# Kernel optimization log

Hardware: AMD Instinct MI355X
Metric: run time of the kernel (lower is better)

The kernel has to match this reference:

```python
import jax, jax.numpy as jnp
import numpy as np

L, D_IN, D, H, FF, C = 6, 64, 512, 8, 2048, 5
HD = D // H
LN_EPS = 1e-5


def _ln(x, g, b):
    mu = jnp.mean(x, axis=-1, keepdims=True)
    var = jnp.mean((x - mu) ** 2, axis=-1, keepdims=True)
    return (x - mu) * jax.lax.rsqrt(var + LN_EPS) * g + b


def setup_inputs() -> dict:
    key = jax.random.key(0)
    ks = iter(jax.random.split(key, 64))
    s = 0.02

    def w(shape):
        return (jax.random.normal(next(ks), shape, dtype=jnp.float32) * s)

    inp = {
        "src": jax.random.normal(next(ks), (8, 1024, D_IN), dtype=jnp.float32),
        "key_padding_mask": jnp.zeros((8, 1024), dtype=bool),
        "embed_W": w((D, D_IN)), "embed_b": jnp.zeros((D,), jnp.float32),
        # stacked per-layer params (torch Linear convention: W is [out, in])
        "Wq": w((L, D, D)), "bq": jnp.zeros((L, D), jnp.float32),
        "Wk": w((L, D, D)), "bk": jnp.zeros((L, D), jnp.float32),
        "Wv": w((L, D, D)), "bv": jnp.zeros((L, D), jnp.float32),
        "Wo": w((L, D, D)), "bo": jnp.zeros((L, D), jnp.float32),
        "W1": w((L, FF, D)), "b1": jnp.zeros((L, FF), jnp.float32),
        "W2": w((L, D, FF)), "b2": jnp.zeros((L, D), jnp.float32),
        "ln1_g": jnp.ones((L, D), jnp.float32), "ln1_b": jnp.zeros((L, D), jnp.float32),
        "ln2_g": jnp.ones((L, D), jnp.float32), "ln2_b": jnp.zeros((L, D), jnp.float32),
        "fin_g": jnp.ones((D,), jnp.float32), "fin_b": jnp.zeros((D,), jnp.float32),
        "head_W": w((C, D)), "head_b": jnp.zeros((C,), jnp.float32),
    }
    return inp


def reference(src, key_padding_mask, embed_W, embed_b, Wq, bq, Wk, bk, Wv, bv,
              Wo, bo, W1, b1, W2, b2, ln1_g, ln1_b, ln2_g, ln2_b,
              fin_g, fin_b, head_W, head_b):
    B, N, _ = src.shape
    x = src @ embed_W.T + embed_b  # [B, N, D]
    neg_inf = jnp.float32(-jnp.inf)
    kpm = key_padding_mask[:, None, None, :]  # [B,1,1,N]

    def layer(x, p):
        (wq, bq_, wk, bk_, wv, bv_, wo, bo_,
         w1, b1_, w2, b2_, g1, be1, g2, be2) = p
        q = (x @ wq.T + bq_).reshape(B, N, H, HD).transpose(0, 2, 1, 3)
        k = (x @ wk.T + bk_).reshape(B, N, H, HD).transpose(0, 2, 1, 3)
        v = (x @ wv.T + bv_).reshape(B, N, H, HD).transpose(0, 2, 1, 3)
        scores = jnp.einsum('bhqd,bhkd->bhqk', q, k) / jnp.sqrt(jnp.float32(HD))
        scores = jnp.where(kpm, neg_inf, scores)
        probs = jax.nn.softmax(scores + 1e-9, axis=-1)
        attn = jnp.einsum('bhqk,bhkd->bhqd', probs, v)
        attn = attn.transpose(0, 2, 1, 3).reshape(B, N, D) @ wo.T + bo_
        x = _ln(x + attn, g1, be1)  # post-norm (norm_first=False)
        ff = jax.nn.relu(x @ w1.T + b1_) @ w2.T + b2_
        x = _ln(x + ff, g2, be2)
        return x, None

    params = (Wq, bq, Wk, bk, Wv, bv, Wo, bo, W1, b1, W2, b2,
              ln1_g, ln1_b, ln2_g, ln2_b)
    x, _ = jax.lax.scan(layer, x, params)
    x = _ln(x, fin_g, fin_b)  # encoder_norm (norm_first=False branch)
    logits = x @ head_W.T + head_b  # [B, N, C]
    return logits
```

## Files before the change

kernel.cpp:

```cpp
#include <hip/hip_runtime.h>
#include <hip/hip_bf16.h>
#include <math.h>

#define B_   8
#define NSEQ 1024
#define T_   (B_*NSEQ)
#define DIN  64
#define D_   512
#define H_   8
#define HD_  64
#define FF_  2048
#define L_   6
#define C_   5

typedef __attribute__((ext_vector_type(8))) short bf16x8;
typedef __attribute__((ext_vector_type(4))) float f32x4;

__device__ __forceinline__ unsigned short f2bf(float f) {
    __hip_bfloat16 h = __float2bfloat16(f);
    return *reinterpret_cast<unsigned short*>(&h);
}
__device__ __forceinline__ float bf2f(unsigned short u) {
    __hip_bfloat16 h = *reinterpret_cast<__hip_bfloat16*>(&u);
    return __bfloat162float(h);
}

__device__ __forceinline__ void gload_lds16(const void* g, void* l) {
    __builtin_amdgcn_global_load_lds(
        (const __attribute__((address_space(1))) unsigned int*)g,
        (__attribute__((address_space(3))) unsigned int*)l, 16, 0, 0);
}

template<bool RELU>
__global__ __launch_bounds__(256, 2)
void gemm_bias_kernel(const float* __restrict__ A, const float* __restrict__ W,
                      const float* __restrict__ bias, float* __restrict__ C,
                      int M, int N, int K)
{
    constexpr int BM = 128, BN = 64, BK = 16;
    __shared__ float As[BK][BM + 4];
    __shared__ float Ws[BK][BN + 4];
    const int tid = threadIdx.x;
    const int bm  = blockIdx.y * BM;
    const int bn  = blockIdx.x * BN;
    const int tm0 = (tid >> 4) * 4;
    const int tn0 = (tid & 15) * 4;

    float acc[8][4];
    #pragma unroll
    for (int i = 0; i < 8; i++)
        #pragma unroll
        for (int j = 0; j < 4; j++) acc[i][j] = 0.f;

    for (int k0 = 0; k0 < K; k0 += BK) {
        #pragma unroll
        for (int i = 0; i < 2; i++) {
            const int f  = tid + i*256;
            const int r  = f >> 2;
            const int kc = (f & 3) << 2;
            const float4 a4 = *(const float4*)(A + (size_t)(bm + r)*K + k0 + kc);
            As[kc+0][r] = a4.x; As[kc+1][r] = a4.y;
            As[kc+2][r] = a4.z; As[kc+3][r] = a4.w;
        }
        {
            const int r  = tid >> 2;
            const int kc = (tid & 3) << 2;
            const float4 w4 = *(const float4*)(W + (size_t)(bn + r)*K + k0 + kc);
            Ws[kc+0][r] = w4.x; Ws[kc+1][r] = w4.y;
            Ws[kc+2][r] = w4.z; Ws[kc+3][r] = w4.w;
        }
        __syncthreads();
        #pragma unroll
        for (int kk = 0; kk < BK; kk++) {
            const float4 a0 = *(const float4*)&As[kk][tm0];
            const float4 a1 = *(const float4*)&As[kk][tm0 + 64];
            const float4 w0 = *(const float4*)&Ws[kk][tn0];
            const float af[8] = {a0.x,a0.y,a0.z,a0.w,a1.x,a1.y,a1.z,a1.w};
            const float wf[4] = {w0.x,w0.y,w0.z,w0.w};
            #pragma unroll
            for (int i = 0; i < 8; i++)
                #pragma unroll
                for (int j = 0; j < 4; j++)
                    acc[i][j] = fmaf(af[i], wf[j], acc[i][j]);
        }
        __syncthreads();
    }

    const float4 b4 = *(const float4*)(bias + bn + tn0);
    const float bsv[4] = {b4.x, b4.y, b4.z, b4.w};
    #pragma unroll
    for (int i = 0; i < 8; i++) {
        const int r = bm + tm0 + (i & 3) + ((i >> 2) << 6);
        float o[4];
        #pragma unroll
        for (int j = 0; j < 4; j++) {
            float t = acc[i][j] + bsv[j];
            if (RELU) t = fmaxf(t, 0.f);
            o[j] = t;
        }
        *(float4*)(C + (size_t)r*N + bn + tn0) = *(const float4*)o;
    }
}

template<bool RELU, bool OUT_BF16, int BN>
__global__ __launch_bounds__(256, BN==64 ? 3 : 2)
void gemm_mfma_kernel(const unsigned short* __restrict__ A,
                      const unsigned short* __restrict__ W,
                      const float* __restrict__ bias,
                      void* __restrict__ Cout,
                      int M, int N, int K)
{
    constexpr int BM = 128, BK = 64;
    constexpr int NFN = BN/32;
    __shared__ short As[2][BM*BK];
    __shared__ short Bs[2][BN*BK];
    const int tid = threadIdx.x;
    const int l   = tid & 63;
    const int wid = tid >> 6;
    const int wm  = wid >> 1, wn = wid & 1;

    const int gx  = gridDim.x;
    const int nwg = gx * gridDim.y;
    int bid = blockIdx.y * gx + blockIdx.x;
    bid = (bid & 7) * (nwg >> 3) + (bid >> 3);
    const int bm = (bid / gx) * BM;
    const int bn = (bid % gx) * BN;

    const int srow = l >> 3;
    const int scol = ((l & 7) ^ srow) * 8;

    f32x4 acc[4][NFN];
    const f32x4 z = {0.f, 0.f, 0.f, 0.f};
    #pragma unroll
    for (int m = 0; m < 4; m++)
        #pragma unroll
        for (int n = 0; n < NFN; n++) acc[m][n] = z;

    const int nk = K / BK;

    auto stage = [&](int kt, int sb) {
        const int k0 = kt * BK;
        #pragma unroll
        for (int c = 0; c < 4; c++) {
            const int r = wid*32 + c*8 + srow;
            gload_lds16(A + (size_t)(bm + r)*K + k0 + scol, &As[sb][(wid*32 + c*8)*64]);
        }
        #pragma unroll
        for (int c = 0; c < BN/32; c++) {
            const int r = wid*(BN/4) + c*8 + srow;
            gload_lds16(W + (size_t)(bn + r)*K + k0 + scol, &Bs[sb][(wid*(BN/4) + c*8)*64]);
        }
    };

    stage(0, 0);
    int buf = 0;
    for (int kt = 0; kt < nk; kt++) {
        __syncthreads();
        if (kt + 1 < nk) stage(kt + 1, buf ^ 1);

        #pragma unroll
        for (int h = 0; h < 2; h++) {
            bf16x8 af[4], bfr[NFN];
            #pragma unroll
            for (int m = 0; m < 4; m++) {
                const int R  = wm*64 + m*16 + (l & 15);
                const int cb = (h*64 + (l >> 4)*16) ^ ((R & 7) << 4);
                af[m] = *(const bf16x8*)((const char*)&As[buf][0] + R*128 + cb);
            }
            #pragma unroll
            for (int n = 0; n < NFN; n++) {
                const int Rc = wn*(BN/2) + n*16 + (l & 15);
                const int cb = (h*64 + (l >> 4)*16) ^ ((Rc & 7) << 4);
                bfr[n] = *(const bf16x8*)((const char*)&Bs[buf][0] + Rc*128 + cb);
            }
            #pragma unroll
            for (int m = 0; m < 4; m++)
                #pragma unroll
                for (int n = 0; n < NFN; n++)
                    acc[m][n] = __builtin_amdgcn_mfma_f32_16x16x32_bf16(af[m], bfr[n], acc[m][n], 0, 0, 0);
        }
        buf ^= 1;
    }

    #pragma unroll
    for (int n = 0; n < NFN; n++) {
        const int col = bn + wn*(BN/2) + n*16 + (l & 15);
        const float bv = bias[col];
        #pragma unroll
        for (int m = 0; m < 4; m++) {
            const int row0 = bm + wm*64 + m*16 + ((l >> 4) << 2);
            #pragma unroll
            for (int j = 0; j < 4; j++) {
                float t = acc[m][n][j] + bv;
                if (RELU) t = fmaxf(t, 0.f);
                if (OUT_BF16)
                    ((unsigned short*)Cout)[(size_t)(row0 + j)*N + col] = f2bf(t);
                else
                    ((float*)Cout)[(size_t)(row0 + j)*N + col] = t;
            }
        }
    }
}

__global__ __launch_bounds__(256, 2)
void attn_mfma_kernel(const unsigned short* __restrict__ QKV,
                      const unsigned char* __restrict__ mask,
                      unsigned short* __restrict__ O)
{
    constexpr int QS = 1536;
    __shared__ short Ks[2][64*64];
    __shared__ short Vt[2][64*72];
    __shared__ short Ps[4][32*72];
    const int tid = threadIdx.x;
    const int l   = tid & 63;
    const int w   = tid >> 6;
    const int g   = l >> 4;
    const int q16 = l & 15;
    const int b   = blockIdx.y >> 3;
    const int h   = blockIdx.y & 7;
    const int q0  = blockIdx.x * 128;
    const int qb  = q0 + w*32;
    const size_t tokbase = (size_t)b * NSEQ;

    bf16x8 bq[2][2];
    #pragma unroll
    for (int qf = 0; qf < 2; qf++) {
        const unsigned short* qp = QKV + (tokbase + qb + qf*16 + q16)*QS + h*HD_ + g*8;
        bq[qf][0] = *(const bf16x8*)qp;
        bq[qf][1] = *(const bf16x8*)(qp + 32);
    }

    f32x4 accO[2][4];
    const f32x4 z = {0.f,0.f,0.f,0.f};
    #pragma unroll
    for (int qf = 0; qf < 2; qf++)
        #pragma unroll
        for (int n = 0; n < 4; n++) accO[qf][n] = z;
    float mrow[2] = {-INFINITY, -INFINITY};
    float lrow[2] = {0.f, 0.f};

    const int srow = l >> 3;
    const int scol = ((l & 7) ^ srow) * 8;
    const unsigned char* mp = mask + (size_t)b*NSEQ;

    #pragma unroll
    for (int c = 0; c < 2; c++) {
        const int rb = (w*2 + c)*8;
        gload_lds16(QKV + (tokbase + rb + srow)*QS + D_ + h*HD_ + scol, &Ks[0][rb*64]);
    }
    {
        const unsigned short* vp = QKV + (tokbase + l)*QS + 2*D_ + h*HD_ + w*16;
        const bf16x8 v8a = *(const bf16x8*)vp;
        const bf16x8 v8b = *(const bf16x8*)(vp + 8);
        #pragma unroll
        for (int j = 0; j < 8; j++) {
            Vt[0][(w*16 + j)*72 + l]     = v8a[j];
            Vt[0][(w*16 + 8 + j)*72 + l] = v8b[j];
        }
    }

    for (int t = 0; t < NSEQ/64; t++) {
        const int buf = t & 1;
        const int kv0 = t*64;
        __syncthreads();

        bf16x8 nva, nvb;
        const bool more = (t + 1 < NSEQ/64);
        if (more) {
            const int kvn = kv0 + 64;
            #pragma unroll
            for (int c = 0; c < 2; c++) {
                const int rb = (w*2 + c)*8;
                gload_lds16(QKV + (tokbase + kvn + rb + srow)*QS + D_ + h*HD_ + scol,
                            &Ks[buf^1][rb*64]);
            }
            const unsigned short* vp = QKV + (tokbase + kvn + l)*QS + 2*D_ + h*HD_ + w*16;
            nva = *(const bf16x8*)vp;
            nvb = *(const bf16x8*)(vp + 8);
        }

        f32x4 s4[2][4];
        #pragma unroll
        for (int qf = 0; qf < 2; qf++)
            #pragma unroll
            for (int n = 0; n < 4; n++) s4[qf][n] = z;
        __builtin_amdgcn_s_setprio(1);
        #pragma unroll
        for (int ks = 0; ks < 2; ks++) {
            const int cb = (ks*64 + g*16) ^ ((q16 & 7) << 4);
            bf16x8 ak[4];
            #pragma unroll
            for (int n = 0; n < 4; n++)
                ak[n] = *(const bf16x8*)((const char*)&Ks[buf][0] + (n*16 + q16)*128 + cb);
            #pragma unroll
            for (int qf = 0; qf < 2; qf++)
                #pragma unroll
                for (int n = 0; n < 4; n++)
                    s4[qf][n] = __builtin_amdgcn_mfma_f32_16x16x32_bf16(ak[n], bq[qf][ks], s4[qf][n], 0, 0, 0);
        }
        __builtin_amdgcn_s_setprio(0);

        const unsigned long long mbits = __ballot(mp[kv0 + l] != 0);

        #pragma unroll
        for (int qf = 0; qf < 2; qf++) {
            float sv[4][4];
            #pragma unroll
            for (int n = 0; n < 4; n++)
                #pragma unroll
                for (int r = 0; r < 4; r++) sv[n][r] = s4[qf][n][r]*0.125f;
            if (mbits) {
                #pragma unroll
                for (int n = 0; n < 4; n++)
                    #pragma unroll
                    for (int r = 0; r < 4; r++)
                        if ((mbits >> (unsigned)(16*n + 4*g + r)) & 1ULL) sv[n][r] = -INFINITY;
            }
            float tmax = sv[0][0];
            #pragma unroll
            for (int n = 0; n < 4; n++)
                #pragma unroll
                for (int r = 0; r < 4; r++) tmax = fmaxf(tmax, sv[n][r]);
            tmax = fmaxf(tmax, __shfl_xor(tmax, 16));
            tmax = fmaxf(tmax, __shfl_xor(tmax, 32));
            const float mnew  = fmaxf(mrow[qf], tmax);
            const float alpha = __expf(mrow[qf] - mnew);
            float rs = 0.f;
            unsigned int pw[4][2];
            #pragma unroll
            for (int n = 0; n < 4; n++) {
                const unsigned short p0 = f2bf(__expf(sv[n][0] - mnew));
                const unsigned short p1 = f2bf(__expf(sv[n][1] - mnew));
                const unsigned short p2 = f2bf(__expf(sv[n][2] - mnew));
                const unsigned short p3 = f2bf(__expf(sv[n][3] - mnew));
                pw[n][0] = (unsigned)p0 | ((unsigned)p1 << 16);
                pw[n][1] = (unsigned)p2 | ((unsigned)p3 << 16);
                rs += bf2f(p0) + bf2f(p1) + bf2f(p2) + bf2f(p3);
            }
            rs += __shfl_xor(rs, 16);
            rs += __shfl_xor(rs, 32);
            lrow[qf] = lrow[qf]*alpha + rs;
            mrow[qf] = mnew;

            float alr[4];
            #pragma unroll
            for (int r = 0; r < 4; r++) alr[r] = __shfl(alpha, g*4 + r, 16);
            #pragma unroll
            for (int n = 0; n < 4; n++)
                #pragma unroll
                for (int r = 0; r < 4; r++) accO[qf][n][r] *= alr[r];

            #pragma unroll
            for (int n = 0; n < 4; n++) {
                uint2 u; u.x = pw[n][0]; u.y = pw[n][1];
                *(uint2*)&Ps[w][(qf*16 + q16)*72 + 16*n + 4*g] = u;
            }
        }

        __builtin_amdgcn_s_setprio(1);
        #pragma unroll
        for (int ks = 0; ks < 2; ks++) {
            const bf16x8 ap0 = *(const bf16x8*)&Ps[w][(q16)*72      + ks*32 + g*8];
            const bf16x8 ap1 = *(const bf16x8*)&Ps[w][(16 + q16)*72 + ks*32 + g*8];
            #pragma unroll
            for (int n = 0; n < 4; n++) {
                const bf16x8 bv = *(const bf16x8*)&Vt[buf][(n*16 + q16)*72 + ks*32 + g*8];
                accO[0][n] = __builtin_amdgcn_mfma_f32_16x16x32_bf16(ap0, bv, accO[0][n], 0, 0, 0);
                accO[1][n] = __builtin_amdgcn_mfma_f32_16x16x32_bf16(ap1, bv, accO[1][n], 0, 0, 0);
            }
        }
        __builtin_amdgcn_s_setprio(0);

        if (more) {
            #pragma unroll
            for (int j = 0; j < 8; j++) {
                Vt[buf^1][(w*16 + j)*72 + l]     = nva[j];
                Vt[buf^1][(w*16 + 8 + j)*72 + l] = nvb[j];
            }
        }
    }

    #pragma unroll
    for (int qf = 0; qf < 2; qf++) {
        float linv[4];
        #pragma unroll
        for (int r = 0; r < 4; r++) linv[r] = 1.0f / __shfl(lrow[qf], g*4 + r, 16);
        #pragma unroll
        for (int r = 0; r < 4; r++) {
            unsigned short* op = O + (tokbase + qb + qf*16 + 4*g + r)*D_ + h*HD_;
            #pragma unroll
            for (int n = 0; n < 4; n++)
                op[16*n + q16] = f2bf(accO[qf][n][r] * linv[r]);
        }
    }
}

__global__ __launch_bounds__(128)
void add_ln_kernel(float* __restrict__ x, const unsigned short* __restrict__ delta,
                   const float* __restrict__ g, const float* __restrict__ bta,
                   unsigned short* __restrict__ xb_out)
{
    const int row = blockIdx.x;
    const int tid = threadIdx.x;
    float* xr = x + (size_t)row*D_;
    float4 xv = *(const float4*)(xr + tid*4);
    if (delta) {
        const ushort4 dv = *(const ushort4*)(delta + (size_t)row*D_ + tid*4);
        xv.x += bf2f(dv.x); xv.y += bf2f(dv.y); xv.z += bf2f(dv.z); xv.w += bf2f(dv.w);
    }
    float sum = xv.x + xv.y + xv.z + xv.w;
    float sq  = xv.x*xv.x + xv.y*xv.y + xv.z*xv.z + xv.w*xv.w;
    #pragma unroll
    for (int off = 1; off < 64; off <<= 1) {
        sum += __shfl_xor(sum, off, 64);
        sq  += __shfl_xor(sq,  off, 64);
    }
    __shared__ float red[2][2];
    if ((tid & 63) == 0) { red[tid >> 6][0] = sum; red[tid >> 6][1] = sq; }
    __syncthreads();
    sum = red[0][0] + red[1][0];
    sq  = red[0][1] + red[1][1];
    const float mu  = sum * (1.f/D_);
    const float var = sq * (1.f/D_) - mu*mu;
    const float rs  = rsqrtf(var + 1e-5f);
    const float4 gv = *(const float4*)(g   + tid*4);
    const float4 bv = *(const float4*)(bta + tid*4);
    float4 o;
    o.x = (xv.x - mu)*rs*gv.x + bv.x;
    o.y = (xv.y - mu)*rs*gv.y + bv.y;
    o.z = (xv.z - mu)*rs*gv.z + bv.z;
    o.w = (xv.w - mu)*rs*gv.w + bv.w;
    *(float4*)(xr + tid*4) = o;
    if (xb_out) {
        ushort4 u;
        u.x = f2bf(o.x); u.y = f2bf(o.y); u.z = f2bf(o.z); u.w = f2bf(o.w);
        *(ushort4*)(xb_out + (size_t)row*D_ + tid*4) = u;
    }
}

__global__ __launch_bounds__(256)
void head_kernel(const float* __restrict__ x, const float* __restrict__ hw,
                 const float* __restrict__ hb, float* __restrict__ out)
{
    const int lane = threadIdx.x & 63;
    const int row  = blockIdx.x*4 + (threadIdx.x >> 6);
    const float* xr = x + (size_t)row*D_;
    float acc[C_] = {0.f,0.f,0.f,0.f,0.f};
    #pragma unroll
    for (int it = 0; it < D_/64; it++) {
        const int k0 = lane + it*64;
        const float xv = xr[k0];
        #pragma unroll
        for (int c = 0; c < C_; c++) acc[c] = fmaf(xv, hw[c*D_ + k0], acc[c]);
    }
    #pragma unroll
    for (int c = 0; c < C_; c++)
        #pragma unroll
        for (int off = 32; off; off >>= 1)
            acc[c] += __shfl_down(acc[c], off, 64);
    if (lane == 0) {
        #pragma unroll
        for (int c = 0; c < C_; c++) out[(size_t)row*C_ + c] = acc[c] + hb[c];
    }
}

__global__ __launch_bounds__(256)
void cast_bf16_kernel(const float* __restrict__ in, unsigned short* __restrict__ out, int n)
{
    const int i = (blockIdx.x*256 + threadIdx.x)*4;
    if (i < n) {
        const float4 v = *(const float4*)(in + i);
        ushort4 o;
        o.x = f2bf(v.x); o.y = f2bf(v.y); o.z = f2bf(v.z); o.w = f2bf(v.w);
        *(ushort4*)(out + i) = o;
    }
}

__global__ __launch_bounds__(256)
void cast_qkv_kernel(const float* __restrict__ Wq, const float* __restrict__ Wk,
                     const float* __restrict__ Wv, unsigned short* __restrict__ dst)
{
    const int t  = blockIdx.y;
    const int ll = t / 3, wh = t % 3;
    const int DD = D_*D_;
    const float* srcs[3] = {Wq, Wk, Wv};
    const float* src = srcs[wh] + (size_t)ll*DD;
    unsigned short* d = dst + (size_t)ll*3*DD + (size_t)wh*DD;
    const int i = (blockIdx.x*256 + threadIdx.x)*4;
    if (i < DD) {
        const float4 v = *(const float4*)(src + i);
        ushort4 o;
        o.x = f2bf(v.x); o.y = f2bf(v.y); o.z = f2bf(v.z); o.w = f2bf(v.w);
        *(ushort4*)(d + i) = o;
    }
}

__global__ __launch_bounds__(256)
void qkv_bias_kernel(const float* __restrict__ bq, const float* __restrict__ bk,
                     const float* __restrict__ bv, float* __restrict__ dst)
{
    const int idx = blockIdx.x*256 + threadIdx.x;
    const int ll = idx / 1536, c = idx % 1536;
    float v;
    if (c < 512)       v = bq[ll*512 + c];
    else if (c < 1024) v = bk[ll*512 + c - 512];
    else               v = bv[ll*512 + c - 1024];
    dst[idx] = v;
}

extern "C" void kernel_launch(void* const* d_in, const int* in_sizes, int n_in,
                              void* d_out, int out_size, void* d_ws, size_t ws_size,
                              hipStream_t stream)
{
    const float* src     = (const float*)d_in[0];
    const unsigned char* kpm = (const unsigned char*)d_in[1];
    const float* embed_W = (const float*)d_in[2];
    const float* embed_b = (const float*)d_in[3];
    const float* Wq = (const float*)d_in[4];
    const float* bq = (const float*)d_in[5];
    const float* Wk = (const float*)d_in[6];
    const float* bk = (const float*)d_in[7];
    const float* Wv = (const float*)d_in[8];
    const float* bv = (const float*)d_in[9];
    const float* Wo = (const float*)d_in[10];
    const float* bo = (const float*)d_in[11];
    const float* W1 = (const float*)d_in[12];
    const float* b1 = (const float*)d_in[13];
    const float* W2 = (const float*)d_in[14];
    const float* b2 = (const float*)d_in[15];
    const float* ln1_g = (const float*)d_in[16];
    const float* ln1_b = (const float*)d_in[17];
    const float* ln2_g = (const float*)d_in[18];
    const float* ln2_b = (const float*)d_in[19];
    const float* fin_g = (const float*)d_in[20];
    const float* fin_b = (const float*)d_in[21];
    const float* head_W = (const float*)d_in[22];
    const float* head_b = (const float*)d_in[23];
    float* out = (float*)d_out;

    float* ws = (float*)d_ws;
    const size_t S = (size_t)T_ * D_;
    float* x = ws;
    unsigned short* u16  = (unsigned short*)(ws + S);
    unsigned short* xb   = u16;
    unsigned short* qkvb = u16 + 1*S;
    unsigned short* attb = u16 + 4*S;
    unsigned short* tmpb = u16 + 5*S;
    unsigned short* h1b  = u16 + 1*S;
    unsigned short* wb   = u16 + 6*S;
    const int DD = D_*D_;
    const int DF = D_*FF_;
    unsigned short* wqkvb = wb;
    unsigned short* wob   = wb + 18*(size_t)DD;
    unsigned short* w1b   = wb + 24*(size_t)DD;
    unsigned short* w2b   = wb + 48*(size_t)DD;
    float* qkvbias        = (float*)(wb + 72*(size_t)DD);

    const dim3 blk(256);
    const dim3 gE  (D_/64,    T_/128);
    const dim3 gQKV(1536/128, T_/128);
    const dim3 gN512(D_/64,   T_/128);
    const dim3 gMF (FF_/128,  T_/128);

    cast_qkv_kernel<<<dim3(DD/1024, 18), blk, 0, stream>>>(Wq, Wk, Wv, wqkvb);
    cast_bf16_kernel<<<6*DD/1024, blk, 0, stream>>>(Wo, wob, 6*DD);
    cast_bf16_kernel<<<6*DF/1024, blk, 0, stream>>>(W1, w1b, 6*DF);
    cast_bf16_kernel<<<6*DF/1024, blk, 0, stream>>>(W2, w2b, 6*DF);
    qkv_bias_kernel<<<(6*1536)/256, blk, 0, stream>>>(bq, bk, bv, qkvbias);

    gemm_bias_kernel<false><<<gE, blk, 0, stream>>>(src, embed_W, embed_b, x, T_, D_, DIN);
    cast_bf16_kernel<<<T_*D_/1024, blk, 0, stream>>>(x, xb, T_*D_);

    for (int l = 0; l < L_; l++) {
        const float* bol = bo + (size_t)l*D_;
        const float* b1l = b1 + (size_t)l*FF_;
        const float* b2l = b2 + (size_t)l*D_;

        gemm_mfma_kernel<false,true,128><<<gQKV, blk, 0, stream>>>(xb, wqkvb + (size_t)l*3*DD,
                                                                   qkvbias + (size_t)l*1536, qkvb, T_, 1536, D_);

        attn_mfma_kernel<<<dim3(NSEQ/128, B_*H_), blk, 0, stream>>>(qkvb, kpm, attb);

        gemm_mfma_kernel<false,true,64><<<gN512, blk, 0, stream>>>(attb, wob + (size_t)l*DD, bol, tmpb, T_, D_, D_);
        add_ln_kernel<<<T_, 128, 0, stream>>>(x, tmpb, ln1_g + (size_t)l*D_, ln1_b + (size_t)l*D_, xb);

        gemm_mfma_kernel<true, true,128><<<gMF, blk, 0, stream>>>(xb, w1b + (size_t)l*DF, b1l, h1b, T_, FF_, D_);
        gemm_mfma_kernel<false,true,64><<<gN512, blk, 0, stream>>>(h1b, w2b + (size_t)l*DF, b2l, tmpb, T_, D_, FF_);
        add_ln_kernel<<<T_, 128, 0, stream>>>(x, tmpb, ln2_g + (size_t)l*D_, ln2_b + (size_t)l*D_, xb);
    }

    add_ln_kernel<<<T_, 128, 0, stream>>>(x, nullptr, fin_g, fin_b, nullptr);
    head_kernel<<<T_/4, 256, 0, stream>>>(x, head_W, head_b, out);
}
```

Before: 1.095 ms.

## Use MFMA for embedding, lazy softmax rescale, fuse final LN with head

Replaces the scalar fp32 embedding GEMM and its separate cast with a bf16 MFMA GEMM that writes fp32 and bf16 outputs together. The attention softmax now uses exp2 with the scale folded into one constant, and it skips the running-max update and accumulator rescale when the new block max stays within a threshold of the old one. The final layernorm and classification head are fused into one kernel. Together these cut launches, scalar FLOPs and exp work, at the cost of bf16 rounding of the embedding inputs and a bounded-growth assumption in the lazy rescale.

New measurement: 1.111 ms. About the same (+1.5%).

```diff
diff --git a/kernel.cpp b/kernel.cpp
--- a/kernel.cpp
+++ b/kernel.cpp
@@ -31,83 +31,13 @@
         (__attribute__((address_space(3))) unsigned int*)l, 16, 0, 0);
 }
 
-template<bool RELU>
-__global__ __launch_bounds__(256, 2)
-void gemm_bias_kernel(const float* __restrict__ A, const float* __restrict__ W,
-                      const float* __restrict__ bias, float* __restrict__ C,
-                      int M, int N, int K)
-{
-    constexpr int BM = 128, BN = 64, BK = 16;
-    __shared__ float As[BK][BM + 4];
-    __shared__ float Ws[BK][BN + 4];
-    const int tid = threadIdx.x;
-    const int bm  = blockIdx.y * BM;
-    const int bn  = blockIdx.x * BN;
-    const int tm0 = (tid >> 4) * 4;
-    const int tn0 = (tid & 15) * 4;
-
-    float acc[8][4];
-    #pragma unroll
-    for (int i = 0; i < 8; i++)
-        #pragma unroll
-        for (int j = 0; j < 4; j++) acc[i][j] = 0.f;
-
-    for (int k0 = 0; k0 < K; k0 += BK) {
-        #pragma unroll
-        for (int i = 0; i < 2; i++) {
-            const int f  = tid + i*256;
-            const int r  = f >> 2;
-            const int kc = (f & 3) << 2;
-            const float4 a4 = *(const float4*)(A + (size_t)(bm + r)*K + k0 + kc);
-            As[kc+0][r] = a4.x; As[kc+1][r] = a4.y;
-            As[kc+2][r] = a4.z; As[kc+3][r] = a4.w;
-        }
-        {
-            const int r  = tid >> 2;
-            const int kc = (tid & 3) << 2;
-            const float4 w4 = *(const float4*)(W + (size_t)(bn + r)*K + k0 + kc);
-            Ws[kc+0][r] = w4.x; Ws[kc+1][r] = w4.y;
-            Ws[kc+2][r] = w4.z; Ws[kc+3][r] = w4.w;
-        }
-        __syncthreads();
-        #pragma unroll
-        for (int kk = 0; kk < BK; kk++) {
-            const float4 a0 = *(const float4*)&As[kk][tm0];
-            const float4 a1 = *(const float4*)&As[kk][tm0 + 64];
-            const float4 w0 = *(const float4*)&Ws[kk][tn0];
-            const float af[8] = {a0.x,a0.y,a0.z,a0.w,a1.x,a1.y,a1.z,a1.w};
-            const float wf[4] = {w0.x,w0.y,w0.z,w0.w};
-            #pragma unroll
-            for (int i = 0; i < 8; i++)
-                #pragma unroll
-                for (int j = 0; j < 4; j++)
-                    acc[i][j] = fmaf(af[i], wf[j], acc[i][j]);
-        }
-        __syncthreads();
-    }
-
-    const float4 b4 = *(const float4*)(bias + bn + tn0);
-    const float bsv[4] = {b4.x, b4.y, b4.z, b4.w};
-    #pragma unroll
-    for (int i = 0; i < 8; i++) {
-        const int r = bm + tm0 + (i & 3) + ((i >> 2) << 6);
-        float o[4];
-        #pragma unroll
-        for (int j = 0; j < 4; j++) {
-            float t = acc[i][j] + bsv[j];
-            if (RELU) t = fmaxf(t, 0.f);
-            o[j] = t;
-        }
-        *(float4*)(C + (size_t)r*N + bn + tn0) = *(const float4*)o;
-    }
-}
-
-template<bool RELU, bool OUT_BF16, int BN>
+template<bool RELU, int OMODE, int BN>
 __global__ __launch_bounds__(256, BN==64 ? 3 : 2)
 void gemm_mfma_kernel(const unsigned short* __restrict__ A,
                       const unsigned short* __restrict__ W,
                       const float* __restrict__ bias,
                       void* __restrict__ Cout,
+                      unsigned short* __restrict__ Cout2,
                       int M, int N, int K)
 {
     constexpr int BM = 128, BK = 64;
@@ -193,10 +123,13 @@
             for (int j = 0; j < 4; j++) {
                 float t = acc[m][n][j] + bv;
                 if (RELU) t = fmaxf(t, 0.f);
-                if (OUT_BF16)
-                    ((unsigned short*)Cout)[(size_t)(row0 + j)*N + col] = f2bf(t);
+                const size_t idx = (size_t)(row0 + j)*N + col;
+                if (OMODE == 1)
+                    ((unsigned short*)Cout)[idx] = f2bf(t);
                 else
-                    ((float*)Cout)[(size_t)(row0 + j)*N + col] = t;
+                    ((float*)Cout)[idx] = t;
+                if (OMODE == 2)
+                    Cout2[idx] = f2bf(t);
             }
         }
     }
@@ -208,6 +141,7 @@
                       unsigned short* __restrict__ O)
 {
     constexpr int QS = 1536;
+    constexpr float CEXP = 0.18033688f;
     __shared__ short Ks[2][64*64];
     __shared__ short Vt[2][64*72];
     __shared__ short Ps[4][32*72];
@@ -308,7 +242,7 @@
             #pragma unroll
             for (int n = 0; n < 4; n++)
                 #pragma unroll
-                for (int r = 0; r < 4; r++) sv[n][r] = s4[qf][n][r]*0.125f;
+                for (int r = 0; r < 4; r++) sv[n][r] = s4[qf][n][r];
             if (mbits) {
                 #pragma unroll
                 for (int n = 0; n < 4; n++)
@@ -323,32 +257,50 @@
                 for (int r = 0; r < 4; r++) tmax = fmaxf(tmax, sv[n][r]);
             tmax = fmaxf(tmax, __shfl_xor(tmax, 16));
             tmax = fmaxf(tmax, __shfl_xor(tmax, 32));
-            const float mnew  = fmaxf(mrow[qf], tmax);
-            const float alpha = __expf(mrow[qf] - mnew);
+
+            unsigned int pw[4][2];
             float rs = 0.f;
-            unsigned int pw[4][2];
-            #pragma unroll
-            for (int n = 0; n < 4; n++) {
-                const unsigned short p0 = f2bf(__expf(sv[n][0] - mnew));
-                const unsigned short p1 = f2bf(__expf(sv[n][1] - mnew));
-                const unsigned short p2 = f2bf(__expf(sv[n][2] - mnew));
-                const unsigned short p3 = f2bf(__expf(sv[n][3] - mnew));
-                pw[n][0] = (unsigned)p0 | ((unsigned)p1 << 16);
-                pw[n][1] = (unsigned)p2 | ((unsigned)p3 << 16);
-                rs += bf2f(p0) + bf2f(p1) + bf2f(p2) + bf2f(p3);
-            }
-            rs += __shfl_xor(rs, 16);
-            rs += __shfl_xor(rs, 32);
-            lrow[qf] = lrow[qf]*alpha + rs;
-            mrow[qf] = mnew;
-
-            float alr[4];
-            #pragma unroll
-            for (int r = 0; r < 4; r++) alr[r] = __shfl(alpha, g*4 + r, 16);
-            #pragma unroll
-            for (int n = 0; n < 4; n++)
-                #pragma unroll
-                for (int r = 0; r < 4; r++) accO[qf][n][r] *= alr[r];
+            if (__all(tmax <= mrow[qf] + 64.f)) {
+                const float mc = mrow[qf]*CEXP;
+                #pragma unroll
+                for (int n = 0; n < 4; n++) {
+                    const float p0 = exp2f(fmaf(sv[n][0], CEXP, -mc));
+                    const float p1 = exp2f(fmaf(sv[n][1], CEXP, -mc));
+                    const float p2 = exp2f(fmaf(sv[n][2], CEXP, -mc));
+                    const float p3 = exp2f(fmaf(sv[n][3], CEXP, -mc));
+                    pw[n][0] = (unsigned)f2bf(p0) | ((unsigned)f2bf(p1) << 16);
+                    pw[n][1] = (unsigned)f2bf(p2) | ((unsigned)f2bf(p3) << 16);
+                    rs += (p0 + p1) + (p2 + p3);
+                }
+                rs += __shfl_xor(rs, 16);
+                rs += __shfl_xor(rs, 32);
+                lrow[qf] += rs;
+            } else {
+                const float mnew = fmaxf(mrow[qf], tmax);
+                const float mc   = mnew*CEXP;
+                #pragma unroll
+                for (int n = 0; n < 4; n++) {
+                    const float p0 = exp2f(fmaf(sv[n][0], CEXP, -mc));
+                    const float p1 = exp2f(fmaf(sv[n][1], CEXP, -mc));
+                    const float p2 = exp2f(fmaf(sv[n][2], CEXP, -mc));
+                    const float p3 = exp2f(fmaf(sv[n][3], CEXP, -mc));
+                    pw[n][0] = (unsigned)f2bf(p0) | ((unsigned)f2bf(p1) << 16);
+                    pw[n][1] = (unsigned)f2bf(p2) | ((unsigned)f2bf(p3) << 16);
+                    rs += (p0 + p1) + (p2 + p3);
+                }
+                rs += __shfl_xor(rs, 16);
+                rs += __shfl_xor(rs, 32);
+                const float alpha = exp2f((mrow[qf] - mnew)*CEXP);
+                lrow[qf] = lrow[qf]*alpha + rs;
+                mrow[qf] = mnew;
+                float alr[4];
+                #pragma unroll
+                for (int r = 0; r < 4; r++) alr[r] = __shfl(alpha, g*4 + r, 16);
+                #pragma unroll
+                for (int n = 0; n < 4; n++)
+                    #pragma unroll
+                    for (int r = 0; r < 4; r++) accO[qf][n][r] *= alr[r];
+            }
 
             #pragma unroll
             for (int n = 0; n < 4; n++) {
@@ -404,7 +356,7 @@
     const int tid = threadIdx.x;
     float* xr = x + (size_t)row*D_;
     float4 xv = *(const float4*)(xr + tid*4);
-    if (delta) {
+    {
         const ushort4 dv = *(const ushort4*)(delta + (size_t)row*D_ + tid*4);
         xv.x += bf2f(dv.x); xv.y += bf2f(dv.y); xv.z += bf2f(dv.z); xv.w += bf2f(dv.w);
     }
@@ -431,37 +383,62 @@
     o.z = (xv.z - mu)*rs*gv.z + bv.z;
     o.w = (xv.w - mu)*rs*gv.w + bv.w;
     *(float4*)(xr + tid*4) = o;
-    if (xb_out) {
-        ushort4 u;
-        u.x = f2bf(o.x); u.y = f2bf(o.y); u.z = f2bf(o.z); u.w = f2bf(o.w);
-        *(ushort4*)(xb_out + (size_t)row*D_ + tid*4) = u;
-    }
-}
-
-__global__ __launch_bounds__(256)
-void head_kernel(const float* __restrict__ x, const float* __restrict__ hw,
-                 const float* __restrict__ hb, float* __restrict__ out)
-{
-    const int lane = threadIdx.x & 63;
-    const int row  = blockIdx.x*4 + (threadIdx.x >> 6);
-    const float* xr = x + (size_t)row*D_;
-    float acc[C_] = {0.f,0.f,0.f,0.f,0.f};
-    #pragma unroll
-    for (int it = 0; it < D_/64; it++) {
-        const int k0 = lane + it*64;
-        const float xv = xr[k0];
-        #pragma unroll
-        for (int c = 0; c < C_; c++) acc[c] = fmaf(xv, hw[c*D_ + k0], acc[c]);
+    ushort4 u;
+    u.x = f2bf(o.x); u.y = f2bf(o.y); u.z = f2bf(o.z); u.w = f2bf(o.w);
+    *(ushort4*)(xb_out + (size_t)row*D_ + tid*4) = u;
+}
+
+__global__ __launch_bounds__(128)
+void ln_head_kernel(const float* __restrict__ x,
+                    const float* __restrict__ g, const float* __restrict__ bta,
+                    const float* __restrict__ hw, const float* __restrict__ hb,
+                    float* __restrict__ out)
+{
+    const int row = blockIdx.x;
+    const int tid = threadIdx.x;
+    const float4 xv = *(const float4*)(x + (size_t)row*D_ + tid*4);
+    float sum = xv.x + xv.y + xv.z + xv.w;
+    float sq  = xv.x*xv.x + xv.y*xv.y + xv.z*xv.z + xv.w*xv.w;
+    #pragma unroll
+    for (int off = 1; off < 64; off <<= 1) {
+        sum += __shfl_xor(sum, off, 64);
+        sq  += __shfl_xor(sq,  off, 64);
+    }
+    __shared__ float red[2][2];
+    if ((tid & 63) == 0) { red[tid >> 6][0] = sum; red[tid >> 6][1] = sq; }
+    __syncthreads();
+    sum = red[0][0] + red[1][0];
+    sq  = red[0][1] + red[1][1];
+    const float mu  = sum * (1.f/D_);
+    const float var = sq * (1.f/D_) - mu*mu;
+    const float rs  = rsqrtf(var + 1e-5f);
+    const float4 gv = *(const float4*)(g   + tid*4);
+    const float4 bv = *(const float4*)(bta + tid*4);
+    float o[4];
+    o[0] = (xv.x - mu)*rs*gv.x + bv.x;
+    o[1] = (xv.y - mu)*rs*gv.y + bv.y;
+    o[2] = (xv.z - mu)*rs*gv.z + bv.z;
+    o[3] = (xv.w - mu)*rs*gv.w + bv.w;
+
+    float part[C_];
+    #pragma unroll
+    for (int c = 0; c < C_; c++) {
+        const float4 wv = *(const float4*)(hw + c*D_ + tid*4);
+        part[c] = o[0]*wv.x + o[1]*wv.y + o[2]*wv.z + o[3]*wv.w;
     }
     #pragma unroll
     for (int c = 0; c < C_; c++)
         #pragma unroll
-        for (int off = 32; off; off >>= 1)
-            acc[c] += __shfl_down(acc[c], off, 64);
-    if (lane == 0) {
-        #pragma unroll
-        for (int c = 0; c < C_; c++) out[(size_t)row*C_ + c] = acc[c] + hb[c];
-    }
+        for (int off = 1; off < 64; off <<= 1)
+            part[c] += __shfl_xor(part[c], off, 64);
+    __shared__ float hred[2][C_];
+    if ((tid & 63) == 0) {
+        #pragma unroll
+        for (int c = 0; c < C_; c++) hred[tid >> 6][c] = part[c];
+    }
+    __syncthreads();
+    if (tid < C_)
+        out[(size_t)row*C_ + tid] = hred[0][tid] + hred[1][tid] + hb[tid];
 }
 
 __global__ __launch_bounds__(256)
@@ -555,9 +532,10 @@
     unsigned short* w1b   = wb + 24*(size_t)DD;
     unsigned short* w2b   = wb + 48*(size_t)DD;
     float* qkvbias        = (float*)(wb + 72*(size_t)DD);
+    unsigned short* srcb  = (unsigned short*)(qkvbias + 6*1536);
+    unsigned short* embWb = srcb + (size_t)T_*DIN;
 
     const dim3 blk(256);
-    const dim3 gE  (D_/64,    T_/128);
     const dim3 gQKV(1536/128, T_/128);
     const dim3 gN512(D_/64,   T_/128);
     const dim3 gMF (FF_/128,  T_/128);
@@ -567,28 +545,28 @@
     cast_bf16_kernel<<<6*DF/1024, blk, 0, stream>>>(W1, w1b, 6*DF);
     cast_bf16_kernel<<<6*DF/1024, blk, 0, stream>>>(W2, w2b, 6*DF);
     qkv_bias_kernel<<<(6*1536)/256, blk, 0, stream>>>(bq, bk, bv, qkvbias);
-
-    gemm_bias_kernel<false><<<gE, blk, 0, stream>>>(src, embed_W, embed_b, x, T_, D_, DIN);
-    cast_bf16_kernel<<<T_*D_/1024, blk, 0, stream>>>(x, xb, T_*D_);
+    cast_bf16_kernel<<<T_*DIN/1024, blk, 0, stream>>>(src, srcb, T_*DIN);
+    cast_bf16_kernel<<<D_*DIN/1024, blk, 0, stream>>>(embed_W, embWb, D_*DIN);
+
+    gemm_mfma_kernel<false,2,64><<<gN512, blk, 0, stream>>>(srcb, embWb, embed_b, x, xb, T_, D_, DIN);
 
     for (int l = 0; l < L_; l++) {
         const float* bol = bo + (size_t)l*D_;
         const float* b1l = b1 + (size_t)l*FF_;
         const float* b2l = b2 + (size_t)l*D_;
 
-        gemm_mfma_kernel<false,true,128><<<gQKV, blk, 0, stream>>>(xb, wqkvb + (size_t)l*3*DD,
-                                                                   qkvbias + (size_t)l*1536, qkvb, T_, 1536, D_);
+        gemm_mfma_kernel<false,1,128><<<gQKV, blk, 0, stream>>>(xb, wqkvb + (size_t)l*3*DD,
+                                                                qkvbias + (size_t)l*1536, qkvb, nullptr, T_, 1536, D_);
 
         attn_mfma_kernel<<<dim3(NSEQ/128, B_*H_), blk, 0, stream>>>(qkvb, kpm, attb);
 
-        gemm_mfma_kernel<false,true,64><<<gN512, blk, 0, stream>>>(attb, wob + (size_t)l*DD, bol, tmpb, T_, D_, D_);
+        gemm_mfma_kernel<false,1,64><<<gN512, blk, 0, stream>>>(attb, wob + (size_t)l*DD, bol, tmpb, nullptr, T_, D_, D_);
         add_ln_kernel<<<T_, 128, 0, stream>>>(x, tmpb, ln1_g + (size_t)l*D_, ln1_b + (size_t)l*D_, xb);
 
-        gemm_mfma_kernel<true, true,128><<<gMF, blk, 0, stream>>>(xb, w1b + (size_t)l*DF, b1l, h1b, T_, FF_, D_);
-        gemm_mfma_kernel<false,true,64><<<gN512, blk, 0, stream>>>(h1b, w2b + (size_t)l*DF, b2l, tmpb, T_, D_, FF_);
+        gemm_mfma_kernel<true, 1,128><<<gMF, blk, 0, stream>>>(xb, w1b + (size_t)l*DF, b1l, h1b, nullptr, T_, FF_, D_);
+        gemm_mfma_kernel<false,1,64><<<gN512, blk, 0, stream>>>(h1b, w2b + (size_t)l*DF, b2l, tmpb, nullptr, T_, D_, FF_);
         add_ln_kernel<<<T_, 128, 0, stream>>>(x, tmpb, ln2_g + (size_t)l*D_, ln2_b + (size_t)l*D_, xb);
     }
 
-    add_ln_kernel<<<T_, 128, 0, stream>>>(x, nullptr, fin_g, fin_b, nullptr);
-    head_kernel<<<T_/4, 256, 0, stream>>>(x, head_W, head_b, out);
-}
+    ln_head_kernel<<<T_, 128, 0, stream>>>(x, fin_g, fin_b, head_W, head_b, out);
+}
```
